# Kernel optimization log

Measured on AMD Instinct MI355X. Metric: run time of the kernel, lower is better.

Reference implementation:

```python
import jax, jax.numpy as jnp
import numpy as np

IDIM, CDIM, NUM_HEADS, N, M = 256, 512, 2, 128, 64
T, BSZ = 64, 128


def setup_inputs() -> dict:
    key = jax.random.key(0)
    ks = jax.random.split(key, 12)
    return {
        "embs": jax.random.normal(ks[0], (T, BSZ, IDIM), jnp.float32),
        "lens": jnp.clip(jax.random.randint(ks[1], (BSZ,), 0, 64), 1, T).astype(jnp.int32),
        "mem_bias": jax.random.normal(ks[2], (N, M), jnp.float32) * 0.05,
        "W_ih": jax.random.normal(ks[3], (4 * CDIM, IDIM + NUM_HEADS * M), jnp.float32) * 0.04,
        "W_hh": jax.random.normal(ks[4], (4 * CDIM, CDIM), jnp.float32) * 0.04,
        "b_ih": jnp.zeros((4 * CDIM,), jnp.float32),
        "b_hh": jnp.zeros((4 * CDIM,), jnp.float32),
        "Wr": jax.random.normal(ks[5], (NUM_HEADS, M + 6, CDIM), jnp.float32) * 0.04,
        "br": jnp.zeros((NUM_HEADS, M + 6), jnp.float32),
        "Ww": jax.random.normal(ks[6], (NUM_HEADS, 3 * M + 6, CDIM), jnp.float32) * 0.04,
        "bw": jnp.zeros((NUM_HEADS, 3 * M + 6), jnp.float32),
        "h0": jax.random.normal(ks[7], (CDIM,), jnp.float32) * 0.05,
        "c0": jax.random.normal(ks[8], (CDIM,), jnp.float32) * 0.05,
        "r0": jax.random.normal(ks[9], (NUM_HEADS, M), jnp.float32) * 0.02,
    }


def _address(mem, k, beta, g, s, gamma, w_prev):
    # mem: (b,N,M)  k:(b,M)  beta,g,gamma:(b,1)  s:(b,3)  w_prev:(b,N)
    beta = jax.nn.softplus(beta)
    g = jax.nn.sigmoid(g)
    s = jax.nn.softmax(s, axis=1)
    gamma = 1.0 + jax.nn.softplus(gamma)
    kk = k + 1e-16
    mm = mem + 1e-16
    dot = jnp.einsum('bnm,bm->bn', mm, kk)
    denom = jnp.linalg.norm(mm, axis=-1) * jnp.linalg.norm(kk, axis=-1, keepdims=True)
    sim = dot / jnp.maximum(denom, 1e-8)  # torch cosine_similarity eps
    wc = jax.nn.softmax(beta * sim, axis=1)
    wg = g * wc + (1.0 - g) * w_prev
    # circular convolution with 3-tap shift kernel: c[i]=s0*w[i-1]+s1*w[i]+s2*w[i+1]
    ww = (s[:, 0:1] * jnp.roll(wg, 1, axis=1)
          + s[:, 1:2] * wg
          + s[:, 2:3] * jnp.roll(wg, -1, axis=1))
    wp = ww ** gamma
    return wp / (jnp.sum(wp, axis=1, keepdims=True) + 1e-16)


def _split5(o):
    return o[:, :M], o[:, M:M + 1], o[:, M + 1:M + 2], o[:, M + 2:M + 5], o[:, M + 5:M + 6]


def _ntm_forward(embs, mem_bias, W_ih, W_hh, b_ih, b_hh, Wr, br, Ww, bw, h0, c0, r0):
    bsz = embs.shape[1]
    mem0 = jnp.broadcast_to(mem_bias, (bsz, N, M))
    reads0 = jnp.broadcast_to(r0[:, None, :], (NUM_HEADS, bsz, M))
    w0 = jnp.zeros((NUM_HEADS, bsz, N), embs.dtype)
    h = jnp.broadcast_to(h0, (bsz, CDIM))
    c = jnp.broadcast_to(c0, (bsz, CDIM))

    def step(carry, emb):
        h, c, mem, rw, wws, reads = carry
        x = jnp.concatenate([emb] + [reads[i] for i in range(NUM_HEADS)], axis=1)
        gates = x @ W_ih.T + h @ W_hh.T + (b_ih + b_hh)
        gi, gf, gg, go = jnp.split(gates, 4, axis=1)  # torch LSTM gate order i,f,g,o
        c = jax.nn.sigmoid(gf) * c + jax.nn.sigmoid(gi) * jnp.tanh(gg)
        h = jax.nn.sigmoid(go) * jnp.tanh(c)
        ctrl = h
        new_reads, new_rw, new_wws = [], [], []
        for hi in range(NUM_HEADS):  # head order: read_i then write_i, writes visible to later heads
            orh = ctrl @ Wr[hi].T + br[hi]
            k, beta, g, s, gamma = _split5(orh)
            w = _address(mem, k, beta, g, s, gamma, rw[hi])
            new_rw.append(w)
            new_reads.append(jnp.einsum('bn,bnm->bm', w, mem))
            owh = ctrl @ Ww[hi].T + bw[hi]
            k2, beta2, g2, s2, gamma2 = _split5(owh)
            e = jax.nn.sigmoid(owh[:, M + 6:2 * M + 6])
            a = owh[:, 2 * M + 6:3 * M + 6]
            w2 = _address(mem, k2, beta2, g2, s2, gamma2, wws[hi])
            mem = mem * (1.0 - w2[:, :, None] * e[:, None, :]) + w2[:, :, None] * a[:, None, :]
            new_wws.append(w2)
        o = jnp.concatenate([ctrl] + new_reads, axis=1)
        carry = (h, c, mem, jnp.stack(new_rw), jnp.stack(new_wws), jnp.stack(new_reads))
        return carry, (o, h, c)

    _, (os_, hs, cs) = jax.lax.scan(step, (h, c, mem0, w0, w0, reads0), embs)
    return os_, hs, cs  # (T,b,cdim+H*M), (T,b,cdim), (T,b,cdim)


def reference(embs, lens, mem_bias, W_ih, W_hh, b_ih, b_hh, Wr, br, Ww, bw, h0, c0, r0):
    os_, hs, cs = _ntm_forward(embs, mem_bias, W_ih, W_hh, b_ih, b_hh, Wr, br, Ww, bw, h0, c0, r0)
    bsz = embs.shape[1]
    bi = jnp.arange(bsz)
    h_fin = hs[lens - 1, bi][None]  # (1,b,cdim) final state at true sequence end
    c_fin = cs[lens - 1, bi][None]
    return os_, h_fin, c_fin
```

## Files before the change

kernel.cpp:

```cpp
#include <hip/hip_runtime.h>
#include <cmath>

#define WS_EMBT  0
#define WS_STATE 2097152
#define WS_C     2179072
#define WS_MEM   2244608
#define WS_RW    3293184
#define WS_WWS   3325952
#define WS_PART  3358720

__device__ __forceinline__ float sigm(float x) { return 1.0f / (1.0f + expf(-x)); }
__device__ __forceinline__ float softplusf(float x) {
    return fmaxf(x, 0.0f) + log1pf(expf(-fabsf(x)));
}

__global__ __launch_bounds__(256) void k_embT(const float* __restrict__ embs,
                                              float* __restrict__ ws)
{
    int f4 = blockIdx.x * 256 + threadIdx.x;
    int k4 = f4 & 63, b = (f4 >> 6) & 127, t = f4 >> 13;
    float4 v = *(const float4*)&embs[(size_t)(t * 128 + b) * 256 + k4 * 4];
    *(float4*)&ws[WS_EMBT + ((size_t)(t * 64 + k4) * 128 + b) * 4] = v;
}

__global__ __launch_bounds__(256) void k_init(float* __restrict__ ws,
                                              const float* __restrict__ mem_bias,
                                              const float* __restrict__ h0,
                                              const float* __restrict__ c0,
                                              const float* __restrict__ r0)
{
    int i = blockIdx.x * 256 + threadIdx.x;
    if (i < 81920) {
        int ks = i >> 9, rem = i & 511, c4 = rem & 3;
        int k = ks * 4 + c4;
        ws[WS_STATE + i] = (ks < 32) ? r0[k] : h0[k - 128];
        return;
    }
    int j = i - 81920;
    if (j < 65536) { ws[WS_C + j] = c0[j >> 7]; return; }
    j -= 65536;
    if (j < 1048576) { ws[WS_MEM + j] = mem_bias[j & 8191]; return; }
    j -= 1048576;
    ws[WS_RW + j] = 0.0f;
}

__global__ __launch_bounds__(256) void k_gates(
    const float* __restrict__ W_ih,
    const float* __restrict__ W_hh,
    const float* __restrict__ ws_c,
    float* __restrict__ partials,
    int t)
{
    const int tx = threadIdx.x;
    const int rt = blockIdx.x >> 3, kz = blockIdx.x & 7;
    const int r0 = rt * 32, k0 = kz * 112;

    __shared__ float w_s[32 * 112];
    const float4* w_s4 = (const float4*)w_s;

#pragma unroll
    for (int it = 0; it < 14; ++it) {
        int f = it * 256 + tx;
        int rl = f / 112, kk = f - rl * 112;
        int r = r0 + rl, kg = k0 + kk;
        w_s[f] = (kg < 384) ? W_ih[r * 384 + kg] : W_hh[r * 512 + (kg - 384)];
    }
    __syncthreads();

    const int lane = tx & 63, half = (tx >> 6) & 1, rowgrp = tx >> 7;
    const int b = half * 64 + lane;
    const float* embsT  = ws_c + WS_EMBT + (size_t)t * 32768;
    const float* stateT = ws_c + WS_STATE;

    float acc[16];
#pragma unroll
    for (int r = 0; r < 16; ++r) acc[r] = 0.f;

    auto ldx = [&](int k4) -> float4 {
        int k4g = kz * 28 + k4;
        const float* src = (k4g < 64) ? (embsT + (size_t)k4g * 512)
                                      : (stateT + (size_t)(k4g - 64) * 512);
        return *(const float4*)&src[b * 4];
    };

    float4 xv = ldx(0);
#pragma unroll 4
    for (int k4 = 0; k4 < 28; ++k4) {
        float4 nxt = (k4 < 27) ? ldx(k4 + 1) : xv;
#pragma unroll
        for (int r = 0; r < 16; ++r) {
            float4 wv = w_s4[(rowgrp * 16 + r) * 28 + k4];
            acc[r] += wv.x * xv.x + wv.y * xv.y + wv.z * xv.z + wv.w * xv.w;
        }
        xv = nxt;
    }
#pragma unroll
    for (int r = 0; r < 16; ++r)
        partials[(size_t)kz * 262144 + (r0 + rowgrp * 16 + r) * 128 + b] = acc[r];
}

__global__ __launch_bounds__(256) void k_lstm(
    const float* __restrict__ partials,
    const float* __restrict__ b_ih,
    const float* __restrict__ b_hh,
    float* __restrict__ ws,
    float* __restrict__ d_out,
    const int* __restrict__ lens,
    int t)
{
    const int tx = threadIdx.x;
    const int half = blockIdx.x & 1, cht = blockIdx.x >> 1;
    const int ch = cht * 4 + (tx >> 6);
    const int lane = tx & 63, b = half * 64 + lane;

    float g4[4];
#pragma unroll
    for (int g = 0; g < 4; ++g) {
        int r = g * 512 + ch;
        float s = b_ih[r] + b_hh[r];
#pragma unroll
        for (int kzq = 0; kzq < 8; ++kzq)
            s += partials[(size_t)kzq * 262144 + r * 128 + b];
        g4[g] = s;
    }
    float* cp = ws + WS_C + ch * 128;
    float c_old = cp[b];
    float c_new = sigm(g4[1]) * c_old + sigm(g4[0]) * tanhf(g4[2]);
    float h_new = sigm(g4[3]) * tanhf(c_new);
    cp[b] = c_new;
    ws[WS_STATE + (32 + (ch >> 2)) * 512 + b * 4 + (ch & 3)] = h_new;
    d_out[((size_t)t * 128 + b) * 640 + ch] = h_new;
    if (lens[b] - 1 == t) {
        d_out[5242880 + b * 512 + ch] = h_new;
        d_out[5308416 + b * 512 + ch] = c_new;
    }
}

__global__ __launch_bounds__(256) void k_proj(
    const float* __restrict__ ws_c,
    const float* __restrict__ Wr,
    const float* __restrict__ Ww,
    float* __restrict__ part2)
{
    const int tx = threadIdx.x;
    const int jt = blockIdx.x >> 3, kz = blockIdx.x & 7;
    const int j0 = jt * 16, k0 = kz * 64;

    __shared__ float w_s[16 * 64];
    const float4* w_s4 = (const float4*)w_s;

#pragma unroll
    for (int it = 0; it < 4; ++it) {
        int f = it * 256 + tx;
        int rl = f >> 6, kk = f & 63;
        int j = j0 + rl;
        float v = 0.f;
        if (j < 536) {
            int hi = j >= 268, q = j - hi * 268;
            v = (q < 70) ? Wr[(hi * 70 + q) * 512 + k0 + kk]
                         : Ww[(hi * 198 + (q - 70)) * 512 + k0 + kk];
        }
        w_s[f] = v;
    }
    __syncthreads();

    const int lane = tx & 63, half = (tx >> 6) & 1, rowgrp = tx >> 7;
    const int b = half * 64 + lane;
    const float* stateT = ws_c + WS_STATE;

    float acc[8];
#pragma unroll
    for (int r = 0; r < 8; ++r) acc[r] = 0.f;

    float4 xv = *(const float4*)&stateT[(32 + kz * 16) * 512 + b * 4];
#pragma unroll 4
    for (int k4 = 0; k4 < 16; ++k4) {
        float4 nxt = (k4 < 15)
            ? *(const float4*)&stateT[(32 + kz * 16 + k4 + 1) * 512 + b * 4] : xv;
#pragma unroll
        for (int r = 0; r < 8; ++r) {
            float4 wv = w_s4[(rowgrp * 8 + r) * 16 + k4];
            acc[r] += wv.x * xv.x + wv.y * xv.y + wv.z * xv.z + wv.w * xv.w;
        }
        xv = nxt;
    }
#pragma unroll
    for (int r = 0; r < 8; ++r) {
        int j = j0 + rowgrp * 8 + r;
        if (j < 536) part2[(size_t)kz * 69632 + b * 544 + j] = acc[r];
    }
}

__global__ __launch_bounds__(256) void k_memops(
    const float* __restrict__ part2,
    const float* __restrict__ br,
    const float* __restrict__ bw,
    float* __restrict__ ws,
    float* __restrict__ d_out,
    int t)
{
    const int b = blockIdx.x;
    const int tx = threadIdx.x;
    const int lx = tx & 127;
    const int grp = tx >> 7;
    const int wid = tx >> 6;

    __shared__ float mem_s[128 * 66];
    __shared__ float proj_s[544];
    __shared__ float wg2_s[2 * 128];
    __shared__ float wf_s[2 * 128];
    __shared__ float red_s[16];
    __shared__ float ea_s[128];
    __shared__ float rvp_s[4 * 66];

    float* memg   = ws + WS_MEM;
    float* stateT = ws + WS_STATE;
    float* rwg    = ws + WS_RW;
    float* wwsg   = ws + WS_WWS;

    for (int j = tx; j < 536; j += 256) {
        int hi = j >= 268, q = j - hi * 268;
        float s = (q < 70) ? br[hi * 70 + q] : bw[hi * 198 + (q - 70)];
#pragma unroll
        for (int kzq = 0; kzq < 8; ++kzq)
            s += part2[(size_t)kzq * 69632 + b * 544 + j];
        proj_s[j] = s;
    }
#pragma unroll
    for (int e = 0; e < 8; ++e) {
        int f4 = e * 256 + tx;
        int n = f4 >> 4, m4 = (f4 & 15) * 4;
        float4 v = *(const float4*)&memg[b * 8192 + f4 * 4];
        *(float2*)&mem_s[n * 66 + m4]     = make_float2(v.x, v.y);
        *(float2*)&mem_s[n * 66 + m4 + 2] = make_float2(v.z, v.w);
    }
    __syncthreads();

    for (int hi = 0; hi < 2; ++hi) {
        const float* p = proj_s + hi * 268 + grp * 70;
        float* wprev_g = (grp == 0 ? rwg : wwsg) + (hi * 128 + b) * 128;

        float beta = softplusf(p[64]);
        float g = sigm(p[65]);
        float s0 = p[66], s1 = p[67], s2 = p[68];
        float sm = fmaxf(s0, fmaxf(s1, s2));
        float e0 = expf(s0 - sm), e1 = expf(s1 - sm), e2 = expf(s2 - sm);
        float sden = e0 + e1 + e2;
        s0 = e0 / sden; s1 = e1 / sden; s2 = e2 / sden;
        float gamma = 1.0f + softplusf(p[69]);

        const float* mrow = mem_s + lx * 66;
        float dot = 0.f, nm = 0.f, nk = 0.f;
#pragma unroll
        for (int m = 0; m < 64; m += 2) {
            float2 kv2 = *(const float2*)&p[m];
            float2 mv2 = *(const float2*)&mrow[m];
            float kx = kv2.x + 1e-16f, ky = kv2.y + 1e-16f;
            float mx = mv2.x + 1e-16f, my = mv2.y + 1e-16f;
            dot += mx * kx + my * ky;
            nm  += mx * mx + my * my;
            nk  += kx * kx + ky * ky;
        }
        float sim = dot / fmaxf(sqrtf(nm) * sqrtf(nk), 1e-8f);
        float z = beta * sim;

        float r = z;
#pragma unroll
        for (int d = 32; d > 0; d >>= 1) r = fmaxf(r, __shfl_xor(r, d));
        if ((tx & 63) == 0) red_s[wid] = r;
        __syncthreads();
        float zmax = fmaxf(red_s[grp * 2], red_s[grp * 2 + 1]);
        float ez = expf(z - zmax);
        r = ez;
#pragma unroll
        for (int d = 32; d > 0; d >>= 1) r += __shfl_xor(r, d);
        if ((tx & 63) == 0) red_s[8 + wid] = r;
        __syncthreads();
        float zsum = red_s[8 + grp * 2] + red_s[8 + grp * 2 + 1];
        float wc = ez / zsum;
        float wgv = g * wc + (1.f - g) * wprev_g[lx];
        wg2_s[grp * 128 + lx] = wgv;
        __syncthreads();
        float wwv = s0 * wg2_s[grp * 128 + ((lx + 127) & 127)] + s1 * wgv
                  + s2 * wg2_s[grp * 128 + ((lx + 1) & 127)];
        float wp = powf(wwv, gamma);
        r = wp;
#pragma unroll
        for (int d = 32; d > 0; d >>= 1) r += __shfl_xor(r, d);
        if ((tx & 63) == 0) red_s[wid] = r;
        __syncthreads();
        float psum = red_s[grp * 2] + red_s[grp * 2 + 1];
        float wfin = wp / (psum + 1e-16f);
        wf_s[grp * 128 + lx] = wfin;
        wprev_g[lx] = wfin;
        __syncthreads();

        {
            int m = tx & 63, p4 = tx >> 6;
            float rv = 0.f;
            const int nb = p4 * 32;
#pragma unroll
            for (int n8 = 0; n8 < 32; ++n8) {
                int n = nb + n8;
                rv += wf_s[n] * mem_s[n * 66 + m];
            }
            rvp_s[p4 * 66 + m] = rv;
        }
        if (tx < 64)        ea_s[tx] = sigm(proj_s[hi * 268 + 140 + tx]);
        else if (tx < 128)  ea_s[tx] = proj_s[hi * 268 + 204 + (tx - 64)];
        __syncthreads();

        if (tx < 64) {
            float rvf = rvp_s[tx] + rvp_s[66 + tx] + rvp_s[132 + tx] + rvp_s[198 + tx];
            stateT[((hi * 64 + tx) >> 2) * 512 + b * 4 + (tx & 3)] = rvf;
            d_out[((size_t)t * 128 + b) * 640 + 512 + hi * 64 + tx] = rvf;
        }
#pragma unroll
        for (int e = 0; e < 16; ++e) {
            int f = e * 256 + tx;
            int n = f >> 5, m2 = (f & 31) * 2;
            float w2 = wf_s[128 + n];
            float2 mv = *(const float2*)&mem_s[n * 66 + m2];
            mv.x = mv.x * (1.f - w2 * ea_s[m2])     + w2 * ea_s[64 + m2];
            mv.y = mv.y * (1.f - w2 * ea_s[m2 + 1]) + w2 * ea_s[65 + m2];
            *(float2*)&mem_s[n * 66 + m2] = mv;
            if (hi == 1) *(float2*)&memg[b * 8192 + f * 2] = mv;
        }
        __syncthreads();
    }
}

extern "C" void kernel_launch(void* const* d_in, const int* in_sizes, int n_in,
                              void* d_out, int out_size, void* d_ws, size_t ws_size,
                              hipStream_t stream)
{
    (void)in_sizes; (void)n_in; (void)out_size; (void)ws_size;
    const float* embs     = (const float*)d_in[0];
    const int*   lens     = (const int*)  d_in[1];
    const float* mem_bias = (const float*)d_in[2];
    const float* W_ih     = (const float*)d_in[3];
    const float* W_hh     = (const float*)d_in[4];
    const float* b_ih     = (const float*)d_in[5];
    const float* b_hh     = (const float*)d_in[6];
    const float* Wr       = (const float*)d_in[7];
    const float* br       = (const float*)d_in[8];
    const float* Ww       = (const float*)d_in[9];
    const float* bw       = (const float*)d_in[10];
    const float* h0       = (const float*)d_in[11];
    const float* c0       = (const float*)d_in[12];
    const float* r0       = (const float*)d_in[13];
    float* out = (float*)d_out;
    float* ws  = (float*)d_ws;
    float* partials = ws + WS_PART;
    float* part2    = ws + WS_PART;

    k_embT<<<2048, 256, 0, stream>>>(embs, ws);
    k_init<<<4928, 256, 0, stream>>>(ws, mem_bias, h0, c0, r0);
    for (int t = 0; t < 64; ++t) {
        k_gates<<<512, 256, 0, stream>>>(W_ih, W_hh, ws, partials, t);
        k_lstm<<<256, 256, 0, stream>>>(partials, b_ih, b_hh, ws, out, lens, t);
        k_proj<<<272, 256, 0, stream>>>(ws, Wr, Ww, part2);
        k_memops<<<128, 256, 0, stream>>>(part2, br, bw, ws, out, t);
    }
}
```

Baseline: 3.084 ms.

## Stage activations in LDS for gates and projection GEMMs with two-batch register tiles

```diff
diff --git a/kernel.cpp b/kernel.cpp
--- a/kernel.cpp
+++ b/kernel.cpp
@@ -9,6 +9,8 @@
 #define WS_WWS   3325952
 #define WS_PART  3358720
 
+#define GATES_LDS_BYTES ((3584 + 14336) * 4)
+
 __device__ __forceinline__ float sigm(float x) { return 1.0f / (1.0f + expf(-x)); }
 __device__ __forceinline__ float softplusf(float x) {
     return fmaxf(x, 0.0f) + log1pf(expf(-fabsf(x)));
@@ -44,59 +46,65 @@
     ws[WS_RW + j] = 0.0f;
 }
 
-__global__ __launch_bounds__(256) void k_gates(
+__global__ void __launch_bounds__(256, 2) k_gates(
     const float* __restrict__ W_ih,
     const float* __restrict__ W_hh,
     const float* __restrict__ ws_c,
     float* __restrict__ partials,
     int t)
 {
+    extern __shared__ float sm[];
+    float4* w_s4 = (float4*)sm;
+    float4* x_s4 = (float4*)(sm + 3584);
+
     const int tx = threadIdx.x;
     const int rt = blockIdx.x >> 3, kz = blockIdx.x & 7;
-    const int r0 = rt * 32, k0 = kz * 112;
-
-    __shared__ float w_s[32 * 112];
-    const float4* w_s4 = (const float4*)w_s;
-
+    const int r0g = rt * 32, k0 = kz * 112;
+
+#pragma unroll
+    for (int it = 0; it < 4; ++it) {
+        int f = it * 256 + tx;
+        if (f < 896) {
+            int rl = f / 28, kq = f - rl * 28;
+            int kg = k0 + kq * 4, r = r0g + rl;
+            float4 v = (kg < 384) ? *(const float4*)&W_ih[r * 384 + kg]
+                                  : *(const float4*)&W_hh[r * 512 + (kg - 384)];
+            w_s4[f] = v;
+        }
+    }
+    const float* embsT  = ws_c + WS_EMBT + (size_t)t * 32768;
+    const float* stateT = ws_c + WS_STATE;
 #pragma unroll
     for (int it = 0; it < 14; ++it) {
         int f = it * 256 + tx;
-        int rl = f / 112, kk = f - rl * 112;
-        int r = r0 + rl, kg = k0 + kk;
-        w_s[f] = (kg < 384) ? W_ih[r * 384 + kg] : W_hh[r * 512 + (kg - 384)];
+        int k4 = f >> 7, b = f & 127;
+        int k4g = kz * 28 + k4;
+        const float* src = (k4g < 64) ? &embsT[(size_t)k4g * 512 + b * 4]
+                                      : &stateT[(size_t)(k4g - 64) * 512 + b * 4];
+        x_s4[f] = *(const float4*)src;
     }
     __syncthreads();
 
-    const int lane = tx & 63, half = (tx >> 6) & 1, rowgrp = tx >> 7;
-    const int b = half * 64 + lane;
-    const float* embsT  = ws_c + WS_EMBT + (size_t)t * 32768;
-    const float* stateT = ws_c + WS_STATE;
-
-    float acc[16];
-#pragma unroll
-    for (int r = 0; r < 16; ++r) acc[r] = 0.f;
-
-    auto ldx = [&](int k4) -> float4 {
-        int k4g = kz * 28 + k4;
-        const float* src = (k4g < 64) ? (embsT + (size_t)k4g * 512)
-                                      : (stateT + (size_t)(k4g - 64) * 512);
-        return *(const float4*)&src[b * 4];
-    };
-
-    float4 xv = ldx(0);
+    const int lane = tx & 63, wid = tx >> 6;
+    const int wr0 = wid * 8;
+    float acc0[8] = {}, acc1[8] = {};
 #pragma unroll 4
     for (int k4 = 0; k4 < 28; ++k4) {
-        float4 nxt = (k4 < 27) ? ldx(k4 + 1) : xv;
-#pragma unroll
-        for (int r = 0; r < 16; ++r) {
-            float4 wv = w_s4[(rowgrp * 16 + r) * 28 + k4];
-            acc[r] += wv.x * xv.x + wv.y * xv.y + wv.z * xv.z + wv.w * xv.w;
-        }
-        xv = nxt;
-    }
-#pragma unroll
-    for (int r = 0; r < 16; ++r)
-        partials[(size_t)kz * 262144 + (r0 + rowgrp * 16 + r) * 128 + b] = acc[r];
+        float4 xv0 = x_s4[k4 * 128 + lane];
+        float4 xv1 = x_s4[k4 * 128 + 64 + lane];
+#pragma unroll
+        for (int r = 0; r < 8; ++r) {
+            float4 wv = w_s4[(wr0 + r) * 28 + k4];
+            acc0[r] += wv.x * xv0.x + wv.y * xv0.y + wv.z * xv0.z + wv.w * xv0.w;
+            acc1[r] += wv.x * xv1.x + wv.y * xv1.y + wv.z * xv1.z + wv.w * xv1.w;
+        }
+    }
+#pragma unroll
+    for (int r = 0; r < 8; ++r) {
+        int row = r0g + wr0 + r;
+        partials[(size_t)kz * 262144 + row * 128 + lane]      = acc0[r];
+        partials[(size_t)kz * 262144 + row * 128 + 64 + lane] = acc1[r];
+    }
 }
 
 __global__ __launch_bounds__(256) void k_lstm(
@@ -142,52 +150,56 @@
     const float* __restrict__ Ww,
     float* __restrict__ part2)
 {
+    __shared__ float w_s[16 * 64];
+    __shared__ float x_s[16 * 128 * 4];
+    float4* w_s4 = (float4*)w_s;
+    float4* x_s4 = (float4*)x_s;
+
     const int tx = threadIdx.x;
     const int jt = blockIdx.x >> 3, kz = blockIdx.x & 7;
     const int j0 = jt * 16, k0 = kz * 64;
-
-    __shared__ float w_s[16 * 64];
-    const float4* w_s4 = (const float4*)w_s;
-
-#pragma unroll
-    for (int it = 0; it < 4; ++it) {
-        int f = it * 256 + tx;
-        int rl = f >> 6, kk = f & 63;
+    const float* stateT = ws_c + WS_STATE;
+
+    {
+        int rl = tx >> 4, kq = tx & 15;
         int j = j0 + rl;
-        float v = 0.f;
+        float4 v = make_float4(0.f, 0.f, 0.f, 0.f);
         if (j < 536) {
             int hi = j >= 268, q = j - hi * 268;
-            v = (q < 70) ? Wr[(hi * 70 + q) * 512 + k0 + kk]
-                         : Ww[(hi * 198 + (q - 70)) * 512 + k0 + kk];
-        }
-        w_s[f] = v;
+            v = (q < 70) ? *(const float4*)&Wr[(hi * 70 + q) * 512 + k0 + kq * 4]
+                         : *(const float4*)&Ww[(hi * 198 + (q - 70)) * 512 + k0 + kq * 4];
+        }
+        w_s4[tx] = v;
+    }
+#pragma unroll
+    for (int it = 0; it < 8; ++it) {
+        int f = it * 256 + tx;
+        int k4 = f >> 7, b = f & 127;
+        x_s4[f] = *(const float4*)&stateT[(size_t)(32 + kz * 16 + k4) * 512 + b * 4];
     }
     __syncthreads();
 
-    const int lane = tx & 63, half = (tx >> 6) & 1, rowgrp = tx >> 7;
-    const int b = half * 64 + lane;
-    const float* stateT = ws_c + WS_STATE;
-
-    float acc[8];
-#pragma unroll
-    for (int r = 0; r < 8; ++r) acc[r] = 0.f;
-
-    float4 xv = *(const float4*)&stateT[(32 + kz * 16) * 512 + b * 4];
+    const int lane = tx & 63, wid = tx >> 6;
+    const int jw0 = wid * 4;
+    float acc0[4] = {}, acc1[4] = {};
 #pragma unroll 4
     for (int k4 = 0; k4 < 16; ++k4) {
-        float4 nxt = (k4 < 15)
-            ? *(const float4*)&stateT[(32 + kz * 16 + k4 + 1) * 512 + b * 4] : xv;
-#pragma unroll
-        for (int r = 0; r < 8; ++r) {
-            float4 wv = w_s4[(rowgrp * 8 + r) * 16 + k4];
-            acc[r] += wv.x * xv.x + wv.y * xv.y + wv.z * xv.z + wv.w * xv.w;
-        }
-        xv = nxt;
-    }
-#pragma unroll
-    for (int r = 0; r < 8; ++r) {
-        int j = j0 + rowgrp * 8 + r;
-        if (j < 536) part2[(size_t)kz * 69632 + b * 544 + j] = acc[r];
+        float4 xv0 = x_s4[k4 * 128 + lane];
+        float4 xv1 = x_s4[k4 * 128 + 64 + lane];
+#pragma unroll
+        for (int r = 0; r < 4; ++r) {
+            float4 wv = w_s4[(jw0 + r) * 16 + k4];
+            acc0[r] += wv.x * xv0.x + wv.y * xv0.y + wv.z * xv0.z + wv.w * xv0.w;
+            acc1[r] += wv.x * xv1.x + wv.y * xv1.y + wv.z * xv1.z + wv.w * xv1.w;
+        }
+    }
+#pragma unroll
+    for (int r = 0; r < 4; ++r) {
+        int j = j0 + jw0 + r;
+        if (j < 536) {
+            part2[(size_t)kz * 69632 + lane * 544 + j]        = acc0[r];
+            part2[(size_t)kz * 69632 + (lane + 64) * 544 + j] = acc1[r];
+        }
     }
 }
 
@@ -354,10 +366,13 @@
     float* partials = ws + WS_PART;
     float* part2    = ws + WS_PART;
 
+    hipFuncSetAttribute(reinterpret_cast<const void*>(&k_gates),
+                        hipFuncAttributeMaxDynamicSharedMemorySize, GATES_LDS_BYTES);
+
     k_embT<<<2048, 256, 0, stream>>>(embs, ws);
     k_init<<<4928, 256, 0, stream>>>(ws, mem_bias, h0, c0, r0);
     for (int t = 0; t < 64; ++t) {
-        k_gates<<<512, 256, 0, stream>>>(W_ih, W_hh, ws, partials, t);
+        k_gates<<<512, 256, GATES_LDS_BYTES, stream>>>(W_ih, W_hh, ws, partials, t);
         k_lstm<<<256, 256, 0, stream>>>(partials, b_ih, b_hh, ws, out, lens, t);
         k_proj<<<272, 256, 0, stream>>>(ws, Wr, Ww, part2);
         k_memops<<<128, 256, 0, stream>>>(part2, br, bw, ws, out, t);
```

New measurement: 2.852 ms. 1.08x faster.
